# Performance work log

Measured on AMD Instinct MI355X. Metric: run time of the kernel, lower is better.

The kernel has to match this reference:

```python
import jax, jax.numpy as jnp
import numpy as np
from jax import lax

SAMPLE_RATE = 0.25
RADIUS = 0.2
MAX_NEIGHBORS = 32  # PyG radius() default max_num_neighbors


def fps(pos, m):
    """Farthest point sampling: returns m indices into pos [N,3]."""
    def step(carry, _):
        min_d, last = carry
        d = jnp.sum((pos - pos[last]) ** 2, axis=-1)
        min_d = jnp.minimum(min_d, d)
        return (min_d, jnp.argmax(min_d)), last
    init = (jnp.full((pos.shape[0],), jnp.inf, pos.dtype), jnp.asarray(0, jnp.int32))
    _, idx = lax.scan(step, init, None, length=m)
    return idx


def setup_inputs() -> dict:
    key = jax.random.key(0)
    ks = jax.random.split(key, 7)
    C_in = 128 + 3  # concat(x_j, pos_j - pos_i)
    x = jax.random.normal(ks[0], (16384, 131), dtype=jnp.float32)
    W1 = jax.random.normal(ks[1], (C_in, 128), dtype=jnp.float32) / np.sqrt(C_in)
    b1 = jnp.zeros((128,), jnp.float32)
    W2 = jax.random.normal(ks[2], (128, 128), dtype=jnp.float32) / np.sqrt(128)
    b2 = jnp.zeros((128,), jnp.float32)
    W3 = jax.random.normal(ks[3], (128, 256), dtype=jnp.float32) / np.sqrt(128)
    b3 = jnp.zeros((256,), jnp.float32)
    return {"x": x, "W1": W1, "b1": b1, "W2": W2, "b2": b2, "W3": W3, "b3": b3}


def reference(x, W1, b1, W2, b2, W3, b3):
    pos = x[:, :3]          # [N,3]
    feat = x[:, 3:]         # [N,C]
    N = x.shape[0]
    M = int(N * SAMPLE_RATE)

    idx = fps(pos, M)                       # [M]
    centers = pos[idx]                      # [M,3]

    # radius-ball neighbor query: K nearest within RADIUS (capped, masked)
    d2 = jnp.sum((centers[:, None, :] - pos[None, :, :]) ** 2, axis=-1)  # [M,N]
    neg_d2, col = lax.top_k(-d2, MAX_NEIGHBORS)                          # [M,K]
    valid = (-neg_d2) <= RADIUS ** 2                                     # [M,K]

    # PointConv message: MLP(concat(x_j, pos_j - pos_i)), max-aggregated
    xj = feat[col]                          # [M,K,C]
    rel = pos[col] - centers[:, None, :]    # [M,K,3]
    h = jnp.concatenate([xj, rel], axis=-1)
    h = jax.nn.relu(h @ W1 + b1)
    h = jax.nn.relu(h @ W2 + b2)
    h = jax.nn.relu(h @ W3 + b3)            # [M,K,256]
    h = jnp.where(valid[..., None], h, -jnp.inf)
    out = jnp.max(h, axis=1)                # [M,256]
    out = jnp.where(jnp.any(valid, axis=1)[:, None], out, 0.0)
    return out
```

## Files before the change

kernel.cpp:

```cpp
#include <hip/hip_runtime.h>
#include <hip/hip_fp16.h>

#define NP 16384
#define MC 4096
#define R2F 0.04f
#define MAXC 256

typedef _Float16 f16x8 __attribute__((ext_vector_type(8)));
typedef float f32x4 __attribute__((ext_vector_type(4)));

__device__ __forceinline__ float sqdist3(float ax, float ay, float az,
                                         float bx, float by, float bz) {
    float dx = ax - bx, dy = ay - by, dz = az - bz;
    return __fadd_rn(__fadd_rn(__fmul_rn(dx, dx), __fmul_rn(dy, dy)), __fmul_rn(dz, dz));
}

__global__ __launch_bounds__(256) void k_prep(const float* __restrict__ x,
    const float* __restrict__ W1, const float* __restrict__ W2, const float* __restrict__ W3,
    float4* __restrict__ pos4, _Float16* __restrict__ w1t,
    _Float16* __restrict__ w2t, _Float16* __restrict__ w3t)
{
    int tid = blockIdx.x * 256 + threadIdx.x;
    if (tid < NP) {
        long b = (long)tid * 131;
        float4 p; p.x = x[b]; p.y = x[b + 1]; p.z = x[b + 2]; p.w = 0.f;
        pos4[tid] = p;
    } else if (tid < NP + 128 * 168) {
        int i = tid - NP; int c = i / 168, k = i % 168;
        w1t[i] = (k < 131) ? (_Float16)W1[k * 128 + c] : (_Float16)0.f;
    } else if (tid < NP + 128 * 168 + 128 * 136) {
        int i = tid - (NP + 128 * 168); int c = i / 136, k = i % 136;
        w2t[i] = (k < 128) ? (_Float16)W2[k * 128 + c] : (_Float16)0.f;
    } else if (tid < NP + 128 * 168 + 128 * 136 + 256 * 136) {
        int i = tid - (NP + 128 * 168 + 128 * 136); int c = i / 136, k = i % 136;
        w3t[i] = (k < 128) ? (_Float16)W3[k * 256 + c] : (_Float16)0.f;
    }
}

__global__ __launch_bounds__(512) void k_fps(const float4* __restrict__ pos4,
                                             float4* __restrict__ centers)
{
    __shared__ unsigned long long s_key[2][8];
    const int t = threadIdx.x;
    const int lane = t & 63;
    const int wv = t >> 6;
    float px[32], py[32], pz[32], md[32];
    #pragma unroll
    for (int i = 0; i < 32; i++) {
        float4 p = pos4[i * 512 + t];
        px[i] = p.x; py[i] = p.y; pz[i] = p.z;
        md[i] = __builtin_inff();
    }
    float4 c0 = pos4[0];
    float cx = c0.x, cy = c0.y, cz = c0.z;
    if (t == 0) centers[0] = make_float4(cx, cy, cz, 0.f);
    for (int m = 0; m < MC - 1; m++) {
        float lv = -1.f; int li = 0;
        #pragma unroll
        for (int i = 0; i < 32; i++) {
            float d = sqdist3(px[i], py[i], pz[i], cx, cy, cz);
            float nmd = fminf(md[i], d);
            md[i] = nmd;
            bool gt = nmd > lv;
            lv = gt ? nmd : lv;
            li = gt ? i : li;
        }
        unsigned long long key =
            ((unsigned long long)__float_as_uint(lv) << 32) |
            (unsigned long long)(unsigned)~(unsigned)(li * 512 + t);
        #pragma unroll
        for (int off = 1; off < 64; off <<= 1) {
            unsigned long long o = __shfl_xor(key, off);
            key = (o > key) ? o : key;
        }
        if (lane == 0) s_key[m & 1][wv] = key;
        __syncthreads();
        key = s_key[m & 1][lane & 7];
        #pragma unroll
        for (int off = 1; off < 8; off <<= 1) {
            unsigned long long o = __shfl_xor(key, off);
            key = (o > key) ? o : key;
        }
        int idx = (int)~(unsigned)(key & 0xffffffffull);
        float4 c4 = pos4[idx];
        cx = c4.x; cy = c4.y; cz = c4.z;
        if (t == 0) centers[m + 1] = make_float4(cx, cy, cz, 0.f);
    }
}

__global__ __launch_bounds__(256) void k_knn(const float4* __restrict__ pos4,
                                             const float4* __restrict__ centers,
                                             int* __restrict__ nbr_cnt,
                                             int* __restrict__ nbr_idx)
{
    __shared__ int s_ci[4][MAXC];
    __shared__ float s_cd[4][MAXC];
    const int t = threadIdx.x, lane = t & 63, wv = t >> 6;
    const int m = blockIdx.x * 4 + wv;
    float4 c = centers[m];
    int base = 0;
    for (int ch = 0; ch < NP / 64; ch++) {
        int p = ch * 64 + lane;
        float4 q = pos4[p];
        float d2 = sqdist3(q.x, q.y, q.z, c.x, c.y, c.z);
        bool pred = (d2 <= R2F);
        unsigned long long mk = __ballot(pred);
        if (pred) {
            int slot = base + (int)__popcll(mk & ((1ull << lane) - 1ull));
            if (slot < MAXC) { s_ci[wv][slot] = p; s_cd[wv][slot] = d2; }
        }
        base += (int)__popcll(mk);
    }
    int cc = min(base, MAXC);
    __syncthreads();
    if (cc <= 32) {
        if (lane < cc) nbr_idx[m * 32 + lane] = s_ci[wv][lane];
        if (lane == 0) nbr_cnt[m] = cc;
    } else {
        int ng = (cc + 63) >> 6;
        for (int g = 0; g < ng; g++) {
            int i = g * 64 + lane;
            if (i < cc) {
                float di = s_cd[wv][i]; int pi = s_ci[wv][i];
                int rank = 0;
                for (int j = 0; j < cc; j++) {
                    float dj = s_cd[wv][j]; int pj = s_ci[wv][j];
                    rank += (dj < di || (dj == di && pj < pi)) ? 1 : 0;
                }
                if (rank < 32) nbr_idx[m * 32 + rank] = pi;
            }
        }
        if (lane == 0) nbr_cnt[m] = 32;
    }
}

__global__ __launch_bounds__(256) void k_mlp(const float* __restrict__ x,
    const float4* __restrict__ pos4, const float4* __restrict__ centers,
    const int* __restrict__ nbr_cnt, const int* __restrict__ nbr_idx,
    const _Float16* __restrict__ w1t, const _Float16* __restrict__ w2t,
    const _Float16* __restrict__ w3t,
    const float* __restrict__ b1, const float* __restrict__ b2, const float* __restrict__ b3,
    float* __restrict__ out)
{
    __shared__ __align__(16) _Float16 sA[64 * 168];
    __shared__ __align__(16) _Float16 sW[256 * 136];
    __shared__ __align__(16) _Float16 sH1[64 * 136];
    __shared__ __align__(16) _Float16 sH2[64 * 136];
    __shared__ float s_pool[4][256];
    __shared__ int s_cnt[2];

    const int t = threadIdx.x, lane = t & 63, wv = t >> 6;
    const int bid = blockIdx.x;

    {
        int r = t >> 2, tsub = t & 3;
        int g = r >> 5, s = r & 31;
        int m = bid * 2 + g;
        int cnt = nbr_cnt[m];
        if (t < 2) s_cnt[t] = nbr_cnt[bid * 2 + t];
        _Float16* row = &sA[r * 168];
        if (s < cnt) {
            int col = nbr_idx[m * 32 + s];
            const float* fx = x + (long)col * 131 + 3;
            for (int k = tsub * 32; k < tsub * 32 + 32; k++) row[k] = (_Float16)fx[k];
            if (tsub == 0) {
                float4 ctr = centers[m];
                float4 pp = pos4[col];
                row[128] = (_Float16)(pp.x - ctr.x);
                row[129] = (_Float16)(pp.y - ctr.y);
                row[130] = (_Float16)(pp.z - ctr.z);
                for (int k = 131; k < 168; k++) row[k] = (_Float16)0.f;
            }
        } else {
            for (int k = tsub * 32; k < tsub * 32 + 32; k++) row[k] = (_Float16)0.f;
            if (tsub == 0) for (int k = 128; k < 168; k++) row[k] = (_Float16)0.f;
        }
    }
    {
        const uint4* src = (const uint4*)w1t; uint4* dst = (uint4*)sW;
        for (int i = t; i < (128 * 168) / 8; i += 256) dst[i] = src[i];
    }
    __syncthreads();

    const int cl = lane & 15;
    const int kgrp = (lane >> 4) * 8;
    const int rsub = (lane >> 4) * 4;
    const int R0 = wv * 16;

    {
        f32x4 acc[8];
        #pragma unroll
        for (int i = 0; i < 8; i++) acc[i] = (f32x4){0.f, 0.f, 0.f, 0.f};
        #pragma unroll
        for (int ks = 0; ks < 5; ks++) {
            int kb = ks * 32 + kgrp;
            f16x8 a = *(const f16x8*)&sA[(R0 + cl) * 168 + kb];
            #pragma unroll
            for (int ct = 0; ct < 8; ct++) {
                f16x8 b = *(const f16x8*)&sW[(ct * 16 + cl) * 168 + kb];
                acc[ct] = __builtin_amdgcn_mfma_f32_16x16x32_f16(a, b, acc[ct], 0, 0, 0);
            }
        }
        #pragma unroll
        for (int ct = 0; ct < 8; ct++) {
            int c = ct * 16 + cl;
            float bb = b1[c];
            #pragma unroll
            for (int v = 0; v < 4; v++) {
                float val = fmaxf(acc[ct][v] + bb, 0.f);
                sH1[(R0 + rsub + v) * 136 + c] = (_Float16)val;
            }
        }
    }
    __syncthreads();
    {
        const uint4* src = (const uint4*)w2t; uint4* dst = (uint4*)sW;
        for (int i = t; i < (128 * 136) / 8; i += 256) dst[i] = src[i];
    }
    __syncthreads();
    {
        f32x4 acc[8];
        #pragma unroll
        for (int i = 0; i < 8; i++) acc[i] = (f32x4){0.f, 0.f, 0.f, 0.f};
        #pragma unroll
        for (int ks = 0; ks < 4; ks++) {
            int kb = ks * 32 + kgrp;
            f16x8 a = *(const f16x8*)&sH1[(R0 + cl) * 136 + kb];
            #pragma unroll
            for (int ct = 0; ct < 8; ct++) {
                f16x8 b = *(const f16x8*)&sW[(ct * 16 + cl) * 136 + kb];
                acc[ct] = __builtin_amdgcn_mfma_f32_16x16x32_f16(a, b, acc[ct], 0, 0, 0);
            }
        }
        #pragma unroll
        for (int ct = 0; ct < 8; ct++) {
            int c = ct * 16 + cl;
            float bb = b2[c];
            #pragma unroll
            for (int v = 0; v < 4; v++) {
                float val = fmaxf(acc[ct][v] + bb, 0.f);
                sH2[(R0 + rsub + v) * 136 + c] = (_Float16)val;
            }
        }
    }
    __syncthreads();
    {
        const uint4* src = (const uint4*)w3t; uint4* dst = (uint4*)sW;
        for (int i = t; i < (256 * 136) / 8; i += 256) dst[i] = src[i];
    }
    __syncthreads();
    {
        f32x4 acc[16];
        #pragma unroll
        for (int i = 0; i < 16; i++) acc[i] = (f32x4){0.f, 0.f, 0.f, 0.f};
        #pragma unroll
        for (int ks = 0; ks < 4; ks++) {
            int kb = ks * 32 + kgrp;
            f16x8 a = *(const f16x8*)&sH2[(R0 + cl) * 136 + kb];
            #pragma unroll
            for (int ct = 0; ct < 16; ct++) {
                f16x8 b = *(const f16x8*)&sW[(ct * 16 + cl) * 136 + kb];
                acc[ct] = __builtin_amdgcn_mfma_f32_16x16x32_f16(a, b, acc[ct], 0, 0, 0);
            }
        }
        int cnt = s_cnt[wv >> 1];
        #pragma unroll
        for (int ct = 0; ct < 16; ct++) {
            int c = ct * 16 + cl;
            float bb = b3[c];
            float p = -__builtin_inff();
            #pragma unroll
            for (int v = 0; v < 4; v++) {
                int srow = (wv & 1) * 16 + rsub + v;
                float val = fmaxf(acc[ct][v] + bb, 0.f);
                if (srow < cnt) p = fmaxf(p, val);
            }
            p = fmaxf(p, __shfl_xor(p, 16));
            p = fmaxf(p, __shfl_xor(p, 32));
            if (lane < 16) s_pool[wv][ct * 16 + lane] = p;
        }
    }
    __syncthreads();
    {
        float p0 = fmaxf(s_pool[0][t], s_pool[1][t]);
        float p1 = fmaxf(s_pool[2][t], s_pool[3][t]);
        out[(bid * 2 + 0) * 256 + t] = p0;
        out[(bid * 2 + 1) * 256 + t] = p1;
    }
}

extern "C" void kernel_launch(void* const* d_in, const int* in_sizes, int n_in,
                              void* d_out, int out_size, void* d_ws, size_t ws_size,
                              hipStream_t stream)
{
    const float* x  = (const float*)d_in[0];
    const float* W1 = (const float*)d_in[1];
    const float* b1 = (const float*)d_in[2];
    const float* W2 = (const float*)d_in[3];
    const float* b2 = (const float*)d_in[4];
    const float* W3 = (const float*)d_in[5];
    const float* b3 = (const float*)d_in[6];
    float* out = (float*)d_out;

    char* w = (char*)d_ws;
    float4* pos4    = (float4*)(w + 0);
    float4* centers = (float4*)(w + 262144);
    int* nbr_cnt    = (int*)(w + 327680);
    int* nbr_idx    = (int*)(w + 344064);
    _Float16* w1t   = (_Float16*)(w + 868352);
    _Float16* w2t   = (_Float16*)(w + 911360);
    _Float16* w3t   = (_Float16*)(w + 946176);

    k_prep<<<352, 256, 0, stream>>>(x, W1, W2, W3, pos4, w1t, w2t, w3t);
    k_fps<<<1, 512, 0, stream>>>(pos4, centers);
    k_knn<<<1024, 256, 0, stream>>>(pos4, centers, nbr_cnt, nbr_idx);
    k_mlp<<<2048, 256, 0, stream>>>(x, pos4, centers, nbr_cnt, nbr_idx,
                                    w1t, w2t, w3t, b1, b2, b3, out);
}
```

Baseline: 7.286 ms.

## Morton-sort points and skip per-thread FPS updates using bounding-sphere pruning

Adds a Morton-code counting sort (histogram, scan, scatter) so each FPS thread owns 16 spatially contiguous points, then computes a per-thread bounding sphere. A thread skips its distance update whenever the new center is too far away to lower any of its min-distances, and reuses its cached argmax key. FPS grows to 1024 threads with 16 points each, and the tie-break changes to original index order. This targets the serial FPS loop, which likely dominates runtime, at the cost of three extra small kernels and divergent branches.

```diff
diff --git a/kernel.cpp b/kernel.cpp
--- a/kernel.cpp
+++ b/kernel.cpp
@@ -5,6 +5,7 @@
 #define MC 4096
 #define R2F 0.04f
 #define MAXC 256
+#define NBIN 32768
 
 typedef _Float16 f16x8 __attribute__((ext_vector_type(8)));
 typedef float f32x4 __attribute__((ext_vector_type(4)));
@@ -15,10 +16,20 @@
     return __fadd_rn(__fadd_rn(__fmul_rn(dx, dx), __fmul_rn(dy, dy)), __fmul_rn(dz, dz));
 }
 
+__device__ __forceinline__ unsigned morton3(float X, float Y, float Z) {
+    int qx = (int)fminf(31.f, fmaxf(0.f, (X + 4.5f) * (31.f / 9.f)));
+    int qy = (int)fminf(31.f, fmaxf(0.f, (Y + 4.5f) * (31.f / 9.f)));
+    int qz = (int)fminf(31.f, fmaxf(0.f, (Z + 4.5f) * (31.f / 9.f)));
+    unsigned mx = (qx & 1) | ((qx & 2) << 2) | ((qx & 4) << 4) | ((qx & 8) << 6) | ((qx & 16) << 8);
+    unsigned my = (qy & 1) | ((qy & 2) << 2) | ((qy & 4) << 4) | ((qy & 8) << 6) | ((qy & 16) << 8);
+    unsigned mz = (qz & 1) | ((qz & 2) << 2) | ((qz & 4) << 4) | ((qz & 8) << 6) | ((qz & 16) << 8);
+    return mx | (my << 1) | (mz << 2);
+}
+
 __global__ __launch_bounds__(256) void k_prep(const float* __restrict__ x,
     const float* __restrict__ W1, const float* __restrict__ W2, const float* __restrict__ W3,
     float4* __restrict__ pos4, _Float16* __restrict__ w1t,
-    _Float16* __restrict__ w2t, _Float16* __restrict__ w3t)
+    _Float16* __restrict__ w2t, _Float16* __restrict__ w3t, unsigned* __restrict__ hist)
 {
     int tid = blockIdx.x * 256 + threadIdx.x;
     if (tid < NP) {
@@ -34,40 +45,113 @@
     } else if (tid < NP + 128 * 168 + 128 * 136 + 256 * 136) {
         int i = tid - (NP + 128 * 168 + 128 * 136); int c = i / 136, k = i % 136;
         w3t[i] = (k < 128) ? (_Float16)W3[k * 256 + c] : (_Float16)0.f;
-    }
-}
-
-__global__ __launch_bounds__(512) void k_fps(const float4* __restrict__ pos4,
-                                             float4* __restrict__ centers)
-{
-    __shared__ unsigned long long s_key[2][8];
+    } else if (tid < NP + 128 * 168 + 128 * 136 + 256 * 136 + NBIN) {
+        hist[tid - (NP + 128 * 168 + 128 * 136 + 256 * 136)] = 0u;
+    }
+}
+
+__global__ __launch_bounds__(256) void k_hist(const float* __restrict__ x,
+    unsigned* __restrict__ codes, unsigned* __restrict__ hist)
+{
+    int p = blockIdx.x * 256 + threadIdx.x;
+    if (p < NP) {
+        long b = (long)p * 131;
+        unsigned c = morton3(x[b], x[b + 1], x[b + 2]);
+        codes[p] = c;
+        atomicAdd(&hist[c], 1u);
+    }
+}
+
+__global__ __launch_bounds__(1024) void k_scan(unsigned* __restrict__ hist)
+{
+    __shared__ unsigned wsum[1024];
     const int t = threadIdx.x;
-    const int lane = t & 63;
-    const int wv = t >> 6;
-    float px[32], py[32], pz[32], md[32];
+    const int base = t * 32;
+    unsigned loc[32]; unsigned s = 0;
     #pragma unroll
-    for (int i = 0; i < 32; i++) {
-        float4 p = pos4[i * 512 + t];
+    for (int k = 0; k < 32; k++) loc[k] = hist[base + k];
+    #pragma unroll
+    for (int k = 0; k < 32; k++) { unsigned v = loc[k]; loc[k] = s; s += v; }
+    wsum[t] = s;
+    __syncthreads();
+    for (int off = 1; off < 1024; off <<= 1) {
+        unsigned v = (t >= off) ? wsum[t - off] : 0u;
+        __syncthreads();
+        if (t >= off) wsum[t] += v;
+        __syncthreads();
+    }
+    unsigned coff = wsum[t] - s;
+    #pragma unroll
+    for (int k = 0; k < 32; k++) hist[base + k] = loc[k] + coff;
+}
+
+__global__ __launch_bounds__(256) void k_scatter(const float* __restrict__ x,
+    const unsigned* __restrict__ codes, unsigned* __restrict__ hist,
+    float4* __restrict__ pos4s)
+{
+    int p = blockIdx.x * 256 + threadIdx.x;
+    if (p < NP) {
+        unsigned dst = atomicAdd(&hist[codes[p]], 1u);
+        long b = (long)p * 131;
+        pos4s[dst] = make_float4(x[b], x[b + 1], x[b + 2], __uint_as_float(~(unsigned)p));
+    }
+}
+
+__global__ __launch_bounds__(1024, 4) void k_fps(const float4* __restrict__ pos4s,
+                                                 const float4* __restrict__ pos4,
+                                                 float4* __restrict__ centers)
+{
+    __shared__ unsigned long long s_key[2][16];
+    const int t = threadIdx.x, lane = t & 63, wv = t >> 6;
+    float px[16], py[16], pz[16], md[16];
+    unsigned oin[16];
+    float mnx = 1e30f, mxx = -1e30f, mny = 1e30f, mxy = -1e30f, mnz = 1e30f, mxz = -1e30f;
+    #pragma unroll
+    for (int i = 0; i < 16; i++) {
+        float4 p = pos4s[t * 16 + i];
         px[i] = p.x; py[i] = p.y; pz[i] = p.z;
+        oin[i] = __float_as_uint(p.w);
         md[i] = __builtin_inff();
-    }
+        mnx = fminf(mnx, p.x); mxx = fmaxf(mxx, p.x);
+        mny = fminf(mny, p.y); mxy = fmaxf(mxy, p.y);
+        mnz = fminf(mnz, p.z); mxz = fmaxf(mxz, p.z);
+    }
+    const float bcx = 0.5f * (mnx + mxx), bcy = 0.5f * (mny + mxy), bcz = 0.5f * (mnz + mxz);
+    float br2 = 0.f;
+    #pragma unroll
+    for (int i = 0; i < 16; i++) {
+        float dx = px[i] - bcx, dy = py[i] - bcy, dz = pz[i] - bcz;
+        br2 = fmaxf(br2, dx * dx + dy * dy + dz * dz);
+    }
+    const float br = __builtin_sqrtf(br2) * 1.0001f;
+    float thr2 = __builtin_inff();
+    unsigned long long kc = 0ull;
+
     float4 c0 = pos4[0];
     float cx = c0.x, cy = c0.y, cz = c0.z;
     if (t == 0) centers[0] = make_float4(cx, cy, cz, 0.f);
+
     for (int m = 0; m < MC - 1; m++) {
-        float lv = -1.f; int li = 0;
-        #pragma unroll
-        for (int i = 0; i < 32; i++) {
-            float d = sqdist3(px[i], py[i], pz[i], cx, cy, cz);
-            float nmd = fminf(md[i], d);
-            md[i] = nmd;
-            bool gt = nmd > lv;
-            lv = gt ? nmd : lv;
-            li = gt ? i : li;
-        }
-        unsigned long long key =
-            ((unsigned long long)__float_as_uint(lv) << 32) |
-            (unsigned long long)(unsigned)~(unsigned)(li * 512 + t);
+        float ddx = cx - bcx, ddy = cy - bcy, ddz = cz - bcz;
+        float D2 = ddx * ddx + ddy * ddy + ddz * ddz;
+        if (D2 * 0.999f < thr2) {
+            unsigned long long k = 0ull;
+            #pragma unroll
+            for (int i = 0; i < 16; i++) {
+                float d = sqdist3(px[i], py[i], pz[i], cx, cy, cz);
+                float nmd = fminf(md[i], d);
+                md[i] = nmd;
+                unsigned long long ki =
+                    ((unsigned long long)__float_as_uint(nmd) << 32) |
+                    (unsigned long long)oin[i];
+                k = (ki > k) ? ki : k;
+            }
+            kc = k;
+            float lv = __uint_as_float((unsigned)(kc >> 32));
+            float tt = br + 1.0001f * __builtin_sqrtf(lv);
+            thr2 = tt * tt;
+        }
+        unsigned long long key = kc;
         #pragma unroll
         for (int off = 1; off < 64; off <<= 1) {
             unsigned long long o = __shfl_xor(key, off);
@@ -75,13 +159,13 @@
         }
         if (lane == 0) s_key[m & 1][wv] = key;
         __syncthreads();
-        key = s_key[m & 1][lane & 7];
-        #pragma unroll
-        for (int off = 1; off < 8; off <<= 1) {
+        key = s_key[m & 1][lane & 15];
+        #pragma unroll
+        for (int off = 1; off < 16; off <<= 1) {
             unsigned long long o = __shfl_xor(key, off);
             key = (o > key) ? o : key;
         }
-        int idx = (int)~(unsigned)(key & 0xffffffffull);
+        int idx = (int)(~(unsigned)key);
         float4 c4 = pos4[idx];
         cx = c4.x; cy = c4.y; cz = c4.z;
         if (t == 0) centers[m + 1] = make_float4(cx, cy, cz, 0.f);
@@ -310,9 +394,15 @@
     _Float16* w1t   = (_Float16*)(w + 868352);
     _Float16* w2t   = (_Float16*)(w + 911360);
     _Float16* w3t   = (_Float16*)(w + 946176);
-
-    k_prep<<<352, 256, 0, stream>>>(x, W1, W2, W3, pos4, w1t, w2t, w3t);
-    k_fps<<<1, 512, 0, stream>>>(pos4, centers);
+    float4* pos4s   = (float4*)(w + 1015808);
+    unsigned* codes = (unsigned*)(w + 1277952);
+    unsigned* hist  = (unsigned*)(w + 1343488);
+
+    k_prep<<<480, 256, 0, stream>>>(x, W1, W2, W3, pos4, w1t, w2t, w3t, hist);
+    k_hist<<<64, 256, 0, stream>>>(x, codes, hist);
+    k_scan<<<1, 1024, 0, stream>>>(hist);
+    k_scatter<<<64, 256, 0, stream>>>(x, codes, hist, pos4s);
+    k_fps<<<1, 1024, 0, stream>>>(pos4s, pos4, centers);
     k_knn<<<1024, 256, 0, stream>>>(pos4, centers, nbr_cnt, nbr_idx);
     k_mlp<<<2048, 256, 0, stream>>>(x, pos4, centers, nbr_cnt, nbr_idx,
                                     w1t, w2t, w3t, b1, b2, b3, out);
```

After: 10.74 ms. +47.4%, slower.
